# Performance work log

Hardware: AMD Instinct MI355X
Metric: run time of the kernel (lower is better)

The kernel has to match this reference:

```python
import jax, jax.numpy as jnp
import numpy as np

TIME_WEIGHT = 0.1
CURRENT_TIME = 0.0

def setup_inputs() -> dict:
    key = jax.random.key(0)
    k1, k2, k3, k4, k5 = jax.random.split(key, 5)
    B, M, D, C = 131072, 100, 1024, 16
    return {
        "query": jax.random.normal(k1, (B, D), dtype=jnp.float32),
        "context": jax.random.normal(k2, (B, C), dtype=jnp.float32),
        "mem_keys": jax.random.normal(k3, (M, D), dtype=jnp.float32),
        "mem_values": jax.random.normal(k4, (M, D), dtype=jnp.float32),
        "mem_contexts": jax.random.normal(k5, (M, C), dtype=jnp.float32),
        "mem_timestamps": jnp.zeros((M, 1), dtype=jnp.float32),
    }

def reference(query, context, mem_keys, mem_values, mem_contexts, mem_timestamps):
    # content scores: [B, M]
    scores = jnp.einsum('bd,md->bm', query, mem_keys)
    # contextual binding
    scores = scores + 0.5 * jnp.einsum('bc,mc->bm', context, mem_contexts)
    # exponential time-decay bias, broadcast over batch: [M]
    time_decay = jnp.exp(-TIME_WEIGHT * (CURRENT_TIME - mem_timestamps.squeeze(-1)))
    scores = scores + time_decay[None, :]
    attn = jax.nn.softmax(scores, axis=-1)
    return jnp.einsum('bm,md->bd', attn, mem_values)
```

## Files before the change

kernel.cpp:

```cpp
#include <hip/hip_runtime.h>


typedef __attribute__((ext_vector_type(8))) _Float16 f16x8;
typedef __attribute__((ext_vector_type(4))) float f32x4;

constexpr int DQ = 1024, CD = 16, MM = 100, KD = 1056, NT = 7;
constexpr size_t KE = (size_t)112 * KD;

constexpr int QBUF = 16384, KOFF = 32768, KBUF = 7168;
constexpr int VOFF = 16384, VBUF = 16384;
constexpr int LDSZ = 65536;

#define WAITV(n) asm volatile("s_waitcnt vmcnt(" #n ")" ::: "memory")

__device__ __forceinline__ void gl16(const void* g, void* l) {
    __builtin_amdgcn_global_load_lds(
        (const __attribute__((address_space(1))) unsigned int*)g,
        (__attribute__((address_space(3))) unsigned int*)l, 16, 0, 0);
}

__global__ void build_k(const float* __restrict__ mk, const float* __restrict__ mc,
                        _Float16* __restrict__ KH)
{
    int d = blockIdx.x * 64 + threadIdx.x;
    int m = blockIdx.y;
    if (d >= KD) return;
    float x = 0.f;
    if (m < MM) {
        if (d < DQ)            x = mk[(size_t)m * DQ + d];
        else if (d < DQ + CD)  x = 0.5f * mc[(size_t)m * CD + (d - DQ)];
    }
    KH[(size_t)m * KD + d] = (_Float16)x;
}

__global__ void build_vt(const float* __restrict__ mv, _Float16* __restrict__ VT)
{
    int idx = blockIdx.x * 256 + threadIdx.x;
    int d = idx >> 7, m = idx & 127;
    VT[idx] = (m < MM) ? (_Float16)mv[(size_t)m * DQ + d] : (_Float16)0.f;
}

__global__ __launch_bounds__(256, 2)
void epmem_pipe(const float* __restrict__ q, const float* __restrict__ cx,
                const float* __restrict__ ts,
                const _Float16* __restrict__ KH, const _Float16* __restrict__ VT,
                float* __restrict__ out)
{
    __shared__ __align__(16) char lds[LDSZ];

    const int t = threadIdx.x, w = t >> 6, lane = t & 63;
    const int lr = lane & 15, lk = lane >> 4;
    const int row0 = blockIdx.x * 64;

    float dec[NT];
    #pragma unroll
    for (int nt = 0; nt < NT; ++nt) {
        int m = nt * 16 + lr;
        dec[nt] = (m < MM) ? __expf(0.1f * ts[m]) : 0.f;
    }

    auto stageQ = [&](int buf, int ms) {
        char* dst = lds + buf * QBUF;
        #pragma unroll
        for (int i = 0; i < 4; ++i) {
            int s = i * 256 + t;
            int row = s >> 4;
            int logical = (s & 15) ^ (row & 15);
            gl16(q + (size_t)(row0 + row) * DQ + ms * 64 + logical * 4,
                 dst + (i * 256 + w * 64) * 16);
        }
    };
    auto stageQctx = [&](int buf) {
        char* dst = lds + buf * QBUF;
        gl16(cx + (size_t)(row0 + (t >> 2)) * CD + (t & 3) * 4, dst + (w * 64) * 16);
    };
    auto stageK = [&](int buf, int ks) {
        char* dst = lds + KOFF + buf * KBUF;
        for (int i = w; i < 7; i += 4) {
            int s = i * 64 + lane;
            int m = s >> 2;
            int logical = (s & 3) ^ ((m >> 1) & 3);
            gl16(KH + (size_t)m * KD + ks * 32 + logical * 8, dst + (i * 64) * 16);
        }
    };
    auto stageV = [&](int buf, int c) {
        char* dst = lds + VOFF + buf * VBUF;
        #pragma unroll
        for (int i = 0; i < 4; ++i) {
            int s = i * 256 + t;
            int d = s >> 4;
            int logical = (s & 15) ^ (d & 15);
            gl16(VT + (size_t)(c * 64 + d) * 128 + logical * 8,
                 dst + (i * 256 + w * 64) * 16);
        }
    };

    f32x4 acc[NT];
    #pragma unroll
    for (int nt = 0; nt < NT; ++nt) acc[nt] = (f32x4){0.f, 0.f, 0.f, 0.f};

    auto qkStep = [&](const char* qx, const char* qy, const char* kb) {
        f32x4 x = *(const f32x4*)qx, y = *(const f32x4*)qy;
        f16x8 ah, al;
        #pragma unroll
        for (int e = 0; e < 4; ++e) {
            _Float16 h = (_Float16)x[e]; ah[e] = h;     al[e] = (_Float16)(x[e] - (float)h);
            h = (_Float16)y[e];          ah[4 + e] = h; al[4 + e] = (_Float16)(y[e] - (float)h);
        }
        #pragma unroll
        for (int nt = 0; nt < NT; ++nt) {
            int m = nt * 16 + lr;
            f16x8 bh = *(const f16x8*)(kb + ((m << 2) + (lk ^ ((lr >> 1) & 3))) * 16);
            acc[nt] = __builtin_amdgcn_mfma_f32_16x16x32_f16(ah, bh, acc[nt], 0, 0, 0);
            acc[nt] = __builtin_amdgcn_mfma_f32_16x16x32_f16(al, bh, acc[nt], 0, 0, 0);
        }
    };

    stageQ(0, 0);
    stageK(0, 0); stageK(1, 1);
    if (w < 3) { WAITV(2); } else { WAITV(1); }
    __builtin_amdgcn_s_barrier();

    for (int ss = 0; ss < 32; ++ss) {
        const int ms = ss >> 1, h = ss & 1;
        if (h == 0) {
            if (ms + 1 <= 15)   stageQ((ms + 1) & 1, ms + 1);
            else                stageQctx(0);
        }
        if (ss <= 30) stageK((ss + 2) % 3, ss + 2);

        const char* base = lds + (ms & 1) * QBUF + (w * 16 + lr) * 256;
        const int u0 = h * 8 + 2 * lk;
        qkStep(base + ((u0 ^ lr) << 4), base + (((u0 + 1) ^ lr) << 4),
               lds + KOFF + (ss % 3) * KBUF);

        if (h == 0) {
            if (ss == 30) { if (w < 3) { WAITV(3); } else { WAITV(2); } }
            else          { if (w < 3) { WAITV(6); } else { WAITV(5); } }
        } else {
            if (ss == 31) { WAITV(0); }
            else          { if (w < 3) { WAITV(2); } else { WAITV(1); } }
        }
        __builtin_amdgcn_s_barrier();
    }
    {
        f16x8 ah, al;
        if (lk < 2) {
            const char* base = lds + (w * 16 + lr) * 64;
            f32x4 x = *(const f32x4*)(base + (2 * lk) * 16);
            f32x4 y = *(const f32x4*)(base + (2 * lk + 1) * 16);
            #pragma unroll
            for (int e = 0; e < 4; ++e) {
                _Float16 h = (_Float16)x[e]; ah[e] = h;     al[e] = (_Float16)(x[e] - (float)h);
                h = (_Float16)y[e];          ah[4 + e] = h; al[4 + e] = (_Float16)(y[e] - (float)h);
            }
        } else {
            #pragma unroll
            for (int e = 0; e < 8; ++e) { ah[e] = (_Float16)0.f; al[e] = (_Float16)0.f; }
        }
        const char* kb = lds + KOFF + 2 * KBUF;
        #pragma unroll
        for (int nt = 0; nt < NT; ++nt) {
            int m = nt * 16 + lr;
            f16x8 bh = *(const f16x8*)(kb + ((m << 2) + (lk ^ ((lr >> 1) & 3))) * 16);
            acc[nt] = __builtin_amdgcn_mfma_f32_16x16x32_f16(ah, bh, acc[nt], 0, 0, 0);
            acc[nt] = __builtin_amdgcn_mfma_f32_16x16x32_f16(al, bh, acc[nt], 0, 0, 0);
        }
    }
    __syncthreads();

    stageV(0, 0); stageV(1, 1);

    char* Pb = lds + w * 4096;
    {
        float rm[4] = {-3e38f, -3e38f, -3e38f, -3e38f};
        #pragma unroll
        for (int nt = 0; nt < NT; ++nt) {
            int m = nt * 16 + lr;
            #pragma unroll
            for (int r = 0; r < 4; ++r) {
                float s = (m < MM) ? (acc[nt][r] + dec[nt]) : -3e38f;
                acc[nt][r] = s;
                rm[r] = fmaxf(rm[r], s);
            }
        }
        #pragma unroll
        for (int r = 0; r < 4; ++r)
            #pragma unroll
            for (int off = 1; off < 16; off <<= 1)
                rm[r] = fmaxf(rm[r], __shfl_xor(rm[r], off));
        float rs[4] = {0.f, 0.f, 0.f, 0.f};
        #pragma unroll
        for (int nt = 0; nt < NT; ++nt)
            #pragma unroll
            for (int r = 0; r < 4; ++r) {
                float e = __expf(acc[nt][r] - rm[r]);
                acc[nt][r] = e;
                rs[r] += e;
            }
        #pragma unroll
        for (int r = 0; r < 4; ++r)
            #pragma unroll
            for (int off = 1; off < 16; off <<= 1)
                rs[r] += __shfl_xor(rs[r], off);
        #pragma unroll
        for (int r = 0; r < 4; ++r) {
            float inv = 1.f / rs[r];
            int row = 4 * lk + r;
            #pragma unroll
            for (int nt = 0; nt < NT; ++nt)
                *(_Float16*)(Pb + row * 256 + (((nt * 2 + (lr >> 3)) ^ row) & 15) * 16
                             + (lr & 7) * 2) = (_Float16)(acc[nt][r] * inv);
        }
    }
    if (lane < 32) {
        int row = lane >> 1, sl = 14 + (lane & 1);
        uint4 z = {0u, 0u, 0u, 0u};
        *(uint4*)(Pb + row * 256 + ((sl ^ row) & 15) * 16) = z;
    }
    WAITV(4);
    __builtin_amdgcn_s_barrier();

    f16x8 pa[4];
    #pragma unroll
    for (int k4 = 0; k4 < 4; ++k4)
        pa[k4] = *(const f16x8*)(Pb + lr * 256 + (((k4 * 4 + lk) ^ lr) & 15) * 16);

    for (int c = 0; c < 16; ++c) {
        if (c + 2 < 16) stageV((c + 2) % 3, c + 2);
        const char* vb = lds + VOFF + (c % 3) * VBUF;
        f32x4 o0 = {0.f,0.f,0.f,0.f}, o1 = {0.f,0.f,0.f,0.f};
        f32x4 o2 = {0.f,0.f,0.f,0.f}, o3 = {0.f,0.f,0.f,0.f};
        #pragma unroll
        for (int k4 = 0; k4 < 4; ++k4) {
            const char* vb2 = vb + (((k4 * 4 + lk) ^ lr) & 15) * 16;
            f16x8 b0 = *(const f16x8*)(vb2 + lr * 256);
            f16x8 b1 = *(const f16x8*)(vb2 + (16 + lr) * 256);
            f16x8 b2 = *(const f16x8*)(vb2 + (32 + lr) * 256);
            f16x8 b3 = *(const f16x8*)(vb2 + (48 + lr) * 256);
            o0 = __builtin_amdgcn_mfma_f32_16x16x32_f16(pa[k4], b0, o0, 0, 0, 0);
            o1 = __builtin_amdgcn_mfma_f32_16x16x32_f16(pa[k4], b1, o1, 0, 0, 0);
            o2 = __builtin_amdgcn_mfma_f32_16x16x32_f16(pa[k4], b2, o2, 0, 0, 0);
            o3 = __builtin_amdgcn_mfma_f32_16x16x32_f16(pa[k4], b3, o3, 0, 0, 0);
        }
        #pragma unroll
        for (int r = 0; r < 4; ++r) {
            size_t rw = (size_t)(row0 + w * 16 + 4 * lk + r) * DQ + c * 64;
            __builtin_nontemporal_store(o0[r], &out[rw + lr]);
            __builtin_nontemporal_store(o1[r], &out[rw + 16 + lr]);
            __builtin_nontemporal_store(o2[r], &out[rw + 32 + lr]);
            __builtin_nontemporal_store(o3[r], &out[rw + 48 + lr]);
        }
        if (c == 0)       { WAITV(20); }
        else if (c <= 13) { WAITV(36); }
        else if (c == 14) { WAITV(32); }
        if (c < 15) __builtin_amdgcn_s_barrier();
    }
}

extern "C" void kernel_launch(void* const* d_in, const int* in_sizes, int n_in,
                              void* d_out, int out_size, void* d_ws, size_t ws_size,
                              hipStream_t stream) {
    const float* q  = (const float*)d_in[0];
    const float* cx = (const float*)d_in[1];
    const float* mk = (const float*)d_in[2];
    const float* mv = (const float*)d_in[3];
    const float* mc = (const float*)d_in[4];
    const float* ts = (const float*)d_in[5];
    float* out = (float*)d_out;

    _Float16* wsp = (_Float16*)d_ws;
    _Float16* KH = wsp;
    _Float16* VT = wsp + KE;

    const int B = in_sizes[0] / DQ;

    build_k<<<dim3(17, 112), dim3(64), 0, stream>>>(mk, mc, KH);
    build_vt<<<dim3(512), dim3(256), 0, stream>>>(mv, VT);
    epmem_pipe<<<dim3(B / 64), dim3(256), 0, stream>>>(q, cx, ts, KH, VT, out);
}
```

Baseline: 270.3 us.

## Shrink blocks to 32 rows and 2 waves with wider Q stages

Each block now handles 32 query rows with 128 threads instead of 64 rows with 256. Q is staged in 128-column chunks split into four parts across sub-steps, with a 32-way XOR swizzle. LDS drops to 56 KB and the V-stage loop doubles its loads per thread. The vmcnt waits are retuned to match. The aim is more resident blocks per CU and finer-grained scheduling, at the cost of K/V tiles being reloaded by twice as many blocks and of launch bounds that ask for only one block per SIMD.

```diff
diff --git a/kernel.cpp b/kernel.cpp
--- a/kernel.cpp
+++ b/kernel.cpp
@@ -8,8 +8,8 @@
 constexpr size_t KE = (size_t)112 * KD;
 
 constexpr int QBUF = 16384, KOFF = 32768, KBUF = 7168;
-constexpr int VOFF = 16384, VBUF = 16384;
-constexpr int LDSZ = 65536;
+constexpr int VOFF = 8192, VBUF = 16384;
+constexpr int LDSZ = 57344;
 
 #define WAITV(n) asm volatile("s_waitcnt vmcnt(" #n ")" ::: "memory")
 
@@ -40,7 +40,7 @@
     VT[idx] = (m < MM) ? (_Float16)mv[(size_t)m * DQ + d] : (_Float16)0.f;
 }
 
-__global__ __launch_bounds__(256, 2)
+__global__ __launch_bounds__(128, 1)
 void epmem_pipe(const float* __restrict__ q, const float* __restrict__ cx,
                 const float* __restrict__ ts,
                 const _Float16* __restrict__ KH, const _Float16* __restrict__ VT,
@@ -50,7 +50,8 @@
 
     const int t = threadIdx.x, w = t >> 6, lane = t & 63;
     const int lr = lane & 15, lk = lane >> 4;
-    const int row0 = blockIdx.x * 64;
+    const int row0 = blockIdx.x * 32;
+    const int key = (w * 16 + lr) & 31;
 
     float dec[NT];
     #pragma unroll
@@ -59,24 +60,23 @@
         dec[nt] = (m < MM) ? __expf(0.1f * ts[m]) : 0.f;
     }
 
-    auto stageQ = [&](int buf, int ms) {
+    auto stageQpart = [&](int buf, int W, int h) {
         char* dst = lds + buf * QBUF;
         #pragma unroll
-        for (int i = 0; i < 4; ++i) {
-            int s = i * 256 + t;
-            int row = s >> 4;
-            int logical = (s & 15) ^ (row & 15);
-            gl16(q + (size_t)(row0 + row) * DQ + ms * 64 + logical * 4,
-                 dst + (i * 256 + w * 64) * 16);
-        }
-    };
-    auto stageQctx = [&](int buf) {
-        char* dst = lds + buf * QBUF;
-        gl16(cx + (size_t)(row0 + (t >> 2)) * CD + (t & 3) * 4, dst + (w * 64) * 16);
+        for (int j = 2 * h; j < 2 * h + 2; ++j) {
+            int s = j * 128 + t;
+            int row = s >> 5;
+            int logical = (s & 31) ^ (row & 31);
+            gl16(q + (size_t)(row0 + row) * DQ + W * 128 + logical * 4,
+                 dst + (j * 128 + w * 64) * 16);
+        }
+    };
+    auto stageQctx = [&]() {
+        gl16(cx + (size_t)(row0 + (t >> 2)) * CD + (t & 3) * 4, lds + (w * 64) * 16);
     };
     auto stageK = [&](int buf, int ks) {
         char* dst = lds + KOFF + buf * KBUF;
-        for (int i = w; i < 7; i += 4) {
+        for (int i = w; i < 7; i += 2) {
             int s = i * 64 + lane;
             int m = s >> 2;
             int logical = (s & 3) ^ ((m >> 1) & 3);
@@ -86,12 +86,12 @@
     auto stageV = [&](int buf, int c) {
         char* dst = lds + VOFF + buf * VBUF;
         #pragma unroll
-        for (int i = 0; i < 4; ++i) {
-            int s = i * 256 + t;
+        for (int i = 0; i < 8; ++i) {
+            int s = i * 128 + t;
             int d = s >> 4;
             int logical = (s & 15) ^ (d & 15);
             gl16(VT + (size_t)(c * 64 + d) * 128 + logical * 8,
-                 dst + (i * 256 + w * 64) * 16);
+                 dst + (i * 128 + w * 64) * 16);
         }
     };
 
@@ -116,31 +116,29 @@
         }
     };
 
-    stageQ(0, 0);
+    stageQpart(0, 0, 0); stageQpart(0, 0, 1); stageQpart(0, 0, 2); stageQpart(0, 0, 3);
     stageK(0, 0); stageK(1, 1);
-    if (w < 3) { WAITV(2); } else { WAITV(1); }
+    if (w == 0) { WAITV(4); } else { WAITV(3); }
     __builtin_amdgcn_s_barrier();
 
     for (int ss = 0; ss < 32; ++ss) {
-        const int ms = ss >> 1, h = ss & 1;
-        if (h == 0) {
-            if (ms + 1 <= 15)   stageQ((ms + 1) & 1, ms + 1);
-            else                stageQctx(0);
-        }
-        if (ss <= 30) stageK((ss + 2) % 3, ss + 2);
-
-        const char* base = lds + (ms & 1) * QBUF + (w * 16 + lr) * 256;
+        const int ms = ss >> 2, h = ss & 3;
+        if (ss < 28)       stageQpart((ms + 1) & 1, ms + 1, h);
+        else if (ss == 28) stageQctx();
+        if (ss <= 30)      stageK((ss + 2) % 3, ss + 2);
+
+        const char* base = lds + (ms & 1) * QBUF + (w * 16 + lr) * 512;
         const int u0 = h * 8 + 2 * lk;
-        qkStep(base + ((u0 ^ lr) << 4), base + (((u0 + 1) ^ lr) << 4),
+        qkStep(base + ((u0 ^ key) << 4), base + (((u0 + 1) ^ key) << 4),
                lds + KOFF + (ss % 3) * KBUF);
 
-        if (h == 0) {
-            if (ss == 30) { if (w < 3) { WAITV(3); } else { WAITV(2); } }
-            else          { if (w < 3) { WAITV(6); } else { WAITV(5); } }
-        } else {
-            if (ss == 31) { WAITV(0); }
-            else          { if (w < 3) { WAITV(2); } else { WAITV(1); } }
-        }
+        if (ss <= 27) {
+            if (h == 3) { if (w == 0) { WAITV(4); } else { WAITV(3); } }
+            else        { if (w == 0) { WAITV(6); } else { WAITV(5); } }
+        }
+        else if (ss == 28) { if (w == 0) { WAITV(5); } else { WAITV(4); } }
+        else if (ss <= 30) { if (w == 0) { WAITV(4); } else { WAITV(3); } }
+        else               { WAITV(0); }
         __builtin_amdgcn_s_barrier();
     }
     {
@@ -218,7 +216,7 @@
         uint4 z = {0u, 0u, 0u, 0u};
         *(uint4*)(Pb + row * 256 + ((sl ^ row) & 15) * 16) = z;
     }
-    WAITV(4);
+    WAITV(8);
     __builtin_amdgcn_s_barrier();
 
     f16x8 pa[4];
@@ -251,8 +249,8 @@
             __builtin_nontemporal_store(o2[r], &out[rw + 32 + lr]);
             __builtin_nontemporal_store(o3[r], &out[rw + 48 + lr]);
         }
-        if (c == 0)       { WAITV(20); }
-        else if (c <= 13) { WAITV(36); }
+        if (c == 0)       { WAITV(24); }
+        else if (c <= 13) { WAITV(40); }
         else if (c == 14) { WAITV(32); }
         if (c < 15) __builtin_amdgcn_s_barrier();
     }
@@ -277,5 +275,5 @@
 
     build_k<<<dim3(17, 112), dim3(64), 0, stream>>>(mk, mc, KH);
     build_vt<<<dim3(512), dim3(256), 0, stream>>>(mv, VT);
-    epmem_pipe<<<dim3(B / 64), dim3(256), 0, stream>>>(q, cx, ts, KH, VT, out);
-}
+    epmem_pipe<<<dim3(B / 32), dim3(128), 0, stream>>>(q, cx, ts, KH, VT, out);
+}
```

After: 368.0 us. +36.1%, slower.

## Widen PV output chunks to 128 columns with double-buffered V staging

Applied to the files above, without the earlier changes.

Changes the P·V phase from 16 chunks of 64 columns with triple buffering to 8 chunks of 128 columns with double buffering. The second V buffer reuses the Q region at offset 0. Each chunk now issues 8 MFMAs per k-step and stages twice as much V per load. This halves the number of barriers and wait points in the output loop. In exchange, the first chunk must fully land before compute starts, and there is less prefetch depth, which may expose more load latency.

```diff
diff --git a/kernel.cpp b/kernel.cpp
--- a/kernel.cpp
+++ b/kernel.cpp
@@ -8,7 +8,7 @@
 constexpr size_t KE = (size_t)112 * KD;
 
 constexpr int QBUF = 16384, KOFF = 32768, KBUF = 7168;
-constexpr int VOFF = 16384, VBUF = 16384;
+constexpr int V0OFF = 32768, V1OFF = 0;
 constexpr int LDSZ = 65536;
 
 #define WAITV(n) asm volatile("s_waitcnt vmcnt(" #n ")" ::: "memory")
@@ -83,14 +83,13 @@
             gl16(KH + (size_t)m * KD + ks * 32 + logical * 8, dst + (i * 64) * 16);
         }
     };
-    auto stageV = [&](int buf, int c) {
-        char* dst = lds + VOFF + buf * VBUF;
-        #pragma unroll
-        for (int i = 0; i < 4; ++i) {
+    auto stageV = [&](char* dst, int c) {
+        #pragma unroll
+        for (int i = 0; i < 8; ++i) {
             int s = i * 256 + t;
             int d = s >> 4;
             int logical = (s & 15) ^ (d & 15);
-            gl16(VT + (size_t)(c * 64 + d) * 128 + logical * 8,
+            gl16(VT + (size_t)(c * 128 + d) * 128 + logical * 8,
                  dst + (i * 256 + w * 64) * 16);
         }
     };
@@ -169,7 +168,7 @@
     }
     __syncthreads();
 
-    stageV(0, 0); stageV(1, 1);
+    stageV(lds + V0OFF, 0);
 
     char* Pb = lds + w * 4096;
     {
@@ -218,43 +217,39 @@
         uint4 z = {0u, 0u, 0u, 0u};
         *(uint4*)(Pb + row * 256 + ((sl ^ row) & 15) * 16) = z;
     }
-    WAITV(4);
-    __builtin_amdgcn_s_barrier();
 
     f16x8 pa[4];
     #pragma unroll
     for (int k4 = 0; k4 < 4; ++k4)
         pa[k4] = *(const f16x8*)(Pb + lr * 256 + (((k4 * 4 + lk) ^ lr) & 15) * 16);
-
-    for (int c = 0; c < 16; ++c) {
-        if (c + 2 < 16) stageV((c + 2) % 3, c + 2);
-        const char* vb = lds + VOFF + (c % 3) * VBUF;
-        f32x4 o0 = {0.f,0.f,0.f,0.f}, o1 = {0.f,0.f,0.f,0.f};
-        f32x4 o2 = {0.f,0.f,0.f,0.f}, o3 = {0.f,0.f,0.f,0.f};
+    asm volatile("s_waitcnt lgkmcnt(0)" ::: "memory");
+    WAITV(0);
+    __builtin_amdgcn_s_barrier();
+
+    for (int c = 0; c < 8; ++c) {
+        if (c < 7) stageV(lds + ((c & 1) ? V0OFF : V1OFF), c + 1);
+        const char* vb = lds + ((c & 1) ? V1OFF : V0OFF);
+        f32x4 o[8];
+        #pragma unroll
+        for (int n = 0; n < 8; ++n) o[n] = (f32x4){0.f, 0.f, 0.f, 0.f};
         #pragma unroll
         for (int k4 = 0; k4 < 4; ++k4) {
             const char* vb2 = vb + (((k4 * 4 + lk) ^ lr) & 15) * 16;
-            f16x8 b0 = *(const f16x8*)(vb2 + lr * 256);
-            f16x8 b1 = *(const f16x8*)(vb2 + (16 + lr) * 256);
-            f16x8 b2 = *(const f16x8*)(vb2 + (32 + lr) * 256);
-            f16x8 b3 = *(const f16x8*)(vb2 + (48 + lr) * 256);
-            o0 = __builtin_amdgcn_mfma_f32_16x16x32_f16(pa[k4], b0, o0, 0, 0, 0);
-            o1 = __builtin_amdgcn_mfma_f32_16x16x32_f16(pa[k4], b1, o1, 0, 0, 0);
-            o2 = __builtin_amdgcn_mfma_f32_16x16x32_f16(pa[k4], b2, o2, 0, 0, 0);
-            o3 = __builtin_amdgcn_mfma_f32_16x16x32_f16(pa[k4], b3, o3, 0, 0, 0);
-        }
-        #pragma unroll
-        for (int r = 0; r < 4; ++r) {
-            size_t rw = (size_t)(row0 + w * 16 + 4 * lk + r) * DQ + c * 64;
-            __builtin_nontemporal_store(o0[r], &out[rw + lr]);
-            __builtin_nontemporal_store(o1[r], &out[rw + 16 + lr]);
-            __builtin_nontemporal_store(o2[r], &out[rw + 32 + lr]);
-            __builtin_nontemporal_store(o3[r], &out[rw + 48 + lr]);
-        }
-        if (c == 0)       { WAITV(20); }
-        else if (c <= 13) { WAITV(36); }
-        else if (c == 14) { WAITV(32); }
-        if (c < 15) __builtin_amdgcn_s_barrier();
+            #pragma unroll
+            for (int n = 0; n < 8; ++n) {
+                f16x8 bv = *(const f16x8*)(vb2 + (n * 16 + lr) * 256);
+                o[n] = __builtin_amdgcn_mfma_f32_16x16x32_f16(pa[k4], bv, o[n], 0, 0, 0);
+            }
+        }
+        #pragma unroll
+        for (int n = 0; n < 8; ++n) {
+            #pragma unroll
+            for (int r = 0; r < 4; ++r) {
+                size_t rw = (size_t)(row0 + w * 16 + 4 * lk + r) * DQ + c * 128 + n * 16;
+                __builtin_nontemporal_store(o[n][r], &out[rw + lr]);
+            }
+        }
+        if (c < 7) { WAITV(32); __builtin_amdgcn_s_barrier(); }
     }
 }
 
```

Measured after the change: 274.3 us. Within noise of the previous version (+1.5%).
